# Performance work log

Measured on AMD Instinct MI355X. Metric: run time of the kernel, lower is better.

The kernel has to match this reference:

```python
import jax, jax.numpy as jnp
import numpy as np

EPS = 1e-5

def _conv1x1(x, w, b):
    # x: [B,C,H,W], w: [O,C,1,1], b: [O]
    return jnp.einsum('oc,bchw->bohw', w[:, :, 0, 0], x) + b[None, :, None, None]

def _maxpool(x, s):
    return jax.lax.reduce_window(x, -jnp.inf, jax.lax.max,
                                 (1, 1, s, s), (1, 1, s, s), 'VALID')

def _sra(x, gw, gb, tw, tb, pw, pb, ww, wb, scale):
    # embedded-Gaussian non-local block with spatial sub-sampling on phi/g
    B, C, H, W = x.shape
    ic = gw.shape[0]
    g = _maxpool(_conv1x1(x, gw, gb), scale).reshape(B, ic, -1)    # [B,ic,n]
    phi = _maxpool(_conv1x1(x, pw, pb), scale).reshape(B, ic, -1)  # [B,ic,n]
    theta = _conv1x1(x, tw, tb).reshape(B, ic, -1)                 # [B,ic,N]
    f = jnp.einsum('bcn,bcm->bnm', theta, phi)                     # [B,N,n]
    a = jax.nn.softmax(f, axis=-1)
    y = jnp.einsum('bnm,bcm->bcn', a, g).reshape(B, ic, H, W)
    return _conv1x1(y, ww, wb) + x

def _conv_bn(x, w, gamma, beta, mean, var):
    y = jax.lax.conv_general_dilated(x, w, (1, 1), ((1, 1), (1, 1)),
                                     dimension_numbers=('NCHW', 'OIHW', 'NCHW'))
    inv = gamma / jnp.sqrt(var + EPS)
    return y * inv[None, :, None, None] + (beta - mean * inv)[None, :, None, None]

def setup_inputs() -> dict:
    key = jax.random.key(0)
    B, C = 4, 32
    sizes = [96, 48, 24]
    inp = {}
    ks = iter(jax.random.split(key, 64))
    for i, hw in enumerate(sizes):
        inp[f'fea1_{i}'] = jax.random.normal(next(ks), (B, C, hw, hw), jnp.float32)
        inp[f'fea2_{i}'] = jax.random.normal(next(ks), (B, C, hw, hw), jnp.float32)
    for lv in (1, 2, 3):
        for nm in ('g', 't', 'p'):
            inp[f'{nm}{lv}_w'] = jax.random.normal(next(ks), (C, 2 * C, 1, 1), jnp.float32) * 0.05
            inp[f'{nm}{lv}_b'] = jax.random.normal(next(ks), (C,), jnp.float32) * 0.05
        inp[f'w{lv}_w'] = jax.random.normal(next(ks), (2 * C, C, 1, 1), jnp.float32) * 0.05
        inp[f'w{lv}_b'] = jax.random.normal(next(ks), (2 * C,), jnp.float32) * 0.05
        inp[f'c{lv}_w'] = jax.random.normal(next(ks), (C, 2 * C, 3, 3), jnp.float32) * 0.05
        inp[f'bn{lv}_g'] = jax.random.uniform(next(ks), (C,), jnp.float32, 0.5, 1.5)
        inp[f'bn{lv}_b'] = jax.random.normal(next(ks), (C,), jnp.float32) * 0.05
        inp[f'bn{lv}_m'] = jax.random.normal(next(ks), (C,), jnp.float32) * 0.05
        inp[f'bn{lv}_v'] = jax.random.uniform(next(ks), (C,), jnp.float32, 0.5, 1.5)
    return inp

def reference(fea1_0, fea1_1, fea1_2, fea2_0, fea2_1, fea2_2,
              g1_w, g1_b, t1_w, t1_b, p1_w, p1_b, w1_w, w1_b, c1_w, bn1_g, bn1_b, bn1_m, bn1_v,
              g2_w, g2_b, t2_w, t2_b, p2_w, p2_b, w2_w, w2_b, c2_w, bn2_g, bn2_b, bn2_m, bn2_v,
              g3_w, g3_b, t3_w, t3_b, p3_w, p3_b, w3_w, w3_b, c3_w, bn3_g, bn3_b, bn3_m, bn3_v):
    x1 = jnp.concatenate([fea1_0, fea2_0], axis=1)
    x2 = jnp.concatenate([fea1_1, fea2_1], axis=1)
    x3 = jnp.concatenate([fea1_2, fea2_2], axis=1)
    z1 = _sra(x1, g1_w, g1_b, t1_w, t1_b, p1_w, p1_b, w1_w, w1_b, 2)
    z2 = _sra(x2, g2_w, g2_b, t2_w, t2_b, p2_w, p2_b, w2_w, w2_b, 4)
    z3 = _sra(x3, g3_w, g3_b, t3_w, t3_b, p3_w, p3_b, w3_w, w3_b, 8)
    out1 = _conv_bn(z1, c1_w, bn1_g, bn1_b, bn1_m, bn1_v)
    out2 = _conv_bn(z2, c2_w, bn2_g, bn2_b, bn2_m, bn2_v)
    out3 = _conv_bn(z3, c3_w, bn3_g, bn3_b, bn3_m, bn3_v)
    return (out1, out2, out3)
```

## Files before the change

kernel.cpp:

```cpp
#include <hip/hip_runtime.h>
#include <hip/hip_bf16.h>

typedef __hip_bfloat16 bf16;
typedef __attribute__((ext_vector_type(8))) short short8;
typedef __attribute__((ext_vector_type(4))) float floatx4;

__device__ __forceinline__ float b2f(bf16 v) { return __bfloat162float(v); }
__device__ __forceinline__ bf16 f2b(float v) { return __float2bfloat16(v); }
__device__ __forceinline__ float ldv(const void* p, size_t i, bool f32) {
    return f32 ? ((const float*)p)[i] : b2f(((const bf16*)p)[i]);
}
template <bool F32>
__device__ __forceinline__ float ldt(const void* p, size_t i) {
    return F32 ? ((const float*)p)[i] : b2f(((const bf16*)p)[i]);
}
__device__ __forceinline__ float s2f(short s) {
    unsigned int u = ((unsigned int)(unsigned short)s) << 16;
    float f; __builtin_memcpy(&f, &u, 4); return f;
}
__device__ __forceinline__ short f2s(float f) {
    bf16 h = f2b(f); short s; __builtin_memcpy(&s, &h, 2); return s;
}
__device__ __forceinline__ bool uflag(const int* flag) {
    return __builtin_amdgcn_readfirstlane(flag[0]) != 0;
}
#define MFMA16(a, b, c) __builtin_amdgcn_mfma_f32_16x16x32_bf16(a, b, c, 0, 0, 0)

struct Ptrs { const void* p[45]; };

struct Lvl {
    const void *f1, *f2;
    const float *btgp, *wbf, *bfold;
    const bf16 *Wb, *Wt, *Wc3;
    bf16 *th, *g, *p, *phi, *gt, *yp, *z;
    float* lp;
    int N, n, npad, nch, W, s, wp, H, tX, BN;
    size_t outOff;
};

__global__ void k_detect(const void* x, int* flag) {
    __shared__ int cnt;
    if (threadIdx.x == 0) cnt = 0;
    __syncthreads();
    const unsigned short* us = (const unsigned short*)x;
    int local = 0;
    for (int i = threadIdx.x; i < 8192; i += 256) {
        unsigned e = us[2 * i] & 0x7F80u;
        if (e == 0x7F80u || e == 0u) local++;
    }
    atomicAdd(&cnt, local);
    __syncthreads();
    if (threadIdx.x == 0) flag[0] = (cnt >= 8) ? 1 : 0;
}

#define O_BTGP  0
#define O_WBF   96
#define O_BFOLD 160
#define O_WT    192
#define O_WC3   1216
#define O_WB    10432
#define LVS     13504

__global__ void k_prep(Ptrs in, const int* flag, float* __restrict__ wsf)
{
    int lv = blockIdx.y;
    float* base = wsf + (size_t)lv * LVS;
    const int wb0 = 6 + 13 * lv;
    const void* gw  = in.p[wb0 + 0];
    const void* gb  = in.p[wb0 + 1];
    const void* tw  = in.p[wb0 + 2];
    const void* tb  = in.p[wb0 + 3];
    const void* pw  = in.p[wb0 + 4];
    const void* pb  = in.p[wb0 + 5];
    const void* ww  = in.p[wb0 + 6];
    const void* wb  = in.p[wb0 + 7];
    const void* cw  = in.p[wb0 + 8];
    const void* bng = in.p[wb0 + 9];
    const void* bnb = in.p[wb0 + 10];
    const void* bnm = in.p[wb0 + 11];
    const void* bnv = in.p[wb0 + 12];
    bool f32 = flag[0] != 0;
    int gid = blockIdx.x * 256 + threadIdx.x;
    int stride = gridDim.x * 256;

    float* btgp = base + O_BTGP;
    float* wbf = base + O_WBF;
    float* bfold = base + O_BFOLD;
    bf16* Wt = (bf16*)(base + O_WT);
    bf16* Wc3 = (bf16*)(base + O_WC3);
    bf16* Wb = (bf16*)(base + O_WB);

    for (int e = gid; e < 96 * 64; e += stride) {
        int o = e >> 6, k = e & 63;
        float v;
        if (o < 32)      v = ldv(tw, (size_t)o * 64 + k, f32);
        else if (o < 64) v = ldv(gw, (size_t)(o - 32) * 64 + k, f32);
        else             v = ldv(pw, (size_t)(o - 64) * 64 + k, f32);
        Wb[e] = f2b(v);
    }
    for (int e = gid; e < 96; e += stride) {
        float v = (e < 32) ? ldv(tb, e, f32)
                           : (e < 64 ? ldv(gb, e - 32, f32) : ldv(pb, e - 64, f32));
        btgp[e] = v;
    }
    for (int e = gid; e < 64 * 32; e += stride)
        Wt[e] = f2b(ldv(ww, e, f32));
    for (int e = gid; e < 64; e += stride) wbf[e] = ldv(wb, e, f32);
    for (int e = gid; e < 18432; e += stride) {
        int k = e & 31, n = (e >> 5) & 15, ot = (e >> 9) & 1;
        int tap = (e >> 10) % 9, cc = e / 9216;
        int o = ot * 16 + n, c = cc * 32 + k;
        float inv = ldv(bng, o, f32) * rsqrtf(ldv(bnv, o, f32) + 1e-5f);
        Wc3[e] = f2b(ldv(cw, ((size_t)o * 64 + c) * 9 + tap, f32) * inv);
    }
    for (int e = gid; e < 32; e += stride) {
        float inv = ldv(bng, e, f32) * rsqrtf(ldv(bnv, e, f32) + 1e-5f);
        bfold[e] = ldv(bnb, e, f32) - ldv(bnm, e, f32) * inv;
    }
}

template <bool F32>
__device__ __forceinline__ void tgpm_body(const Lvl& P, int rb)
{
    __shared__ __align__(16) bf16 X[64 * 72];
    int tid = threadIdx.x, lane = tid & 63, wv = tid >> 6;
    int quad = lane >> 4, col = lane & 15;
    int row0 = rb * 64;
    int b = row0 / P.N;
    int pix0 = row0 - b * P.N;

#pragma unroll
    for (int it = 0; it < 16; it++) {
        int e = it * 256 + tid;
        int pix = e & 63, c = e >> 6;
        const void* fx = (c < 32) ? P.f1 : P.f2;
        int cc = c & 31;
        float v = ldt<F32>(fx, (size_t)(b * 32 + cc) * P.N + pix0 + pix);
        X[pix * 72 + c] = f2b(v);
    }
    __syncthreads();

    short8 a_lo = *(const short8*)(X + (wv * 16 + col) * 72 + quad * 8);
    short8 a_hi = *(const short8*)(X + (wv * 16 + col) * 72 + 32 + quad * 8);
    const floatx4 zc = {0.f, 0.f, 0.f, 0.f};
#pragma unroll
    for (int ot = 0; ot < 6; ot++) {
        const bf16* wp = P.Wb + (size_t)(ot * 16 + col) * 64 + quad * 8;
        short8 b_lo = *(const short8*)(wp);
        short8 b_hi = *(const short8*)(wp + 32);
        floatx4 acc = MFMA16(a_lo, b_lo, zc);
        acc = MFMA16(a_hi, b_hi, acc);
        float bias = P.btgp[ot * 16 + col];
        bf16* dst = (ot < 2) ? P.th : ((ot < 4) ? P.g : P.p);
        int och = (ot & 1) * 16 + col;
#pragma unroll
        for (int r = 0; r < 4; r++) {
            int pix = row0 + wv * 16 + quad * 4 + r;
            dst[(size_t)pix * 32 + och] = f2b(acc[r] + bias);
        }
    }
}

__global__ void k_tgpm(Lvl a0, Lvl a1, Lvl a2, int s1, int s2, const int* flag)
{
    int bid = blockIdx.x;
    const Lvl P = bid < s1 ? a0 : (bid < s2 ? a1 : a2);
    int rb = bid - (bid < s1 ? 0 : (bid < s2 ? s1 : s2));
    if (uflag(flag)) tgpm_body<true>(P, rb);
    else             tgpm_body<false>(P, rb);
}

__global__ void k_pool(Lvl a0, Lvl a1, Lvl a2, int s1, int s2)
{
    int bid = blockIdx.x;
    const Lvl P = bid < s1 ? a0 : (bid < s2 ? a1 : a2);
    int local = bid - (bid < s1 ? 0 : (bid < s2 ? s1 : s2));
    int gid = local * 256 + threadIdx.x;
    int npad = P.npad;
    if (gid >= 4 * npad * 32) return;
    int c = gid & 31;
    int j = (gid >> 5) % npad;
    int b = gid / (32 * npad);
    float mg = 0.f, mp = 0.f;
    if (j < P.n) {
        int py = j / P.wp, px = j - py * P.wp;
        const int N = P.N;
        mg = -INFINITY; mp = -INFINITY;
        for (int dy = 0; dy < P.s; dy++)
            for (int dx = 0; dx < P.s; dx++) {
                int idx = (py * P.s + dy) * P.W + px * P.s + dx;
                size_t bse = ((size_t)b * N + idx) * 32 + c;
                mg = fmaxf(mg, b2f(P.g[bse]));
                mp = fmaxf(mp, b2f(P.p[bse]));
            }
    }
    P.phi[((size_t)b * npad + j) * 32 + c] = f2b(mp);
    P.gt[((size_t)b * 32 + c) * npad + j] = f2b(mg);
}

__launch_bounds__(256)
__global__ void k_attn(Lvl a0, Lvl a1, Lvl a2, int s1, int s2)
{
    __shared__ __align__(16) bf16 Pt_s[8 * 1152];
    int bid = blockIdx.x;
    const Lvl P = bid < s1 ? a0 : (bid < s2 ? a1 : a2);
    int local = bid - (bid < s1 ? 0 : (bid < s2 ? s1 : s2));
    int rowblocks = P.BN >> 6;
    int c = local / rowblocks;
    int rb = local - c * rowblocks;

    int tid = threadIdx.x, lane = tid & 63, wv = tid >> 6;
    int quad = lane >> 4, col = lane & 15;
    bf16* Pt0 = Pt_s + wv * 2304;
    int row0 = rb * 64;
    int b = row0 / P.N;
    int npad = P.npad;

    int T = npad >> 6, C = P.nch;
    int js = ((T * c) / C) << 6;
    int je = ((T * (c + 1)) / C) << 6;

    short8 ta = *(const short8*)(P.th + (size_t)(row0 + wv * 16 + col) * 32 + quad * 8);
    const bf16* php = P.phi + (size_t)b * npad * 32 + (size_t)col * 32 + quad * 8;
    const bf16* gtp = P.gt + (size_t)b * 32 * npad + (size_t)col * npad + quad * 8;

    floatx4 y0 = {0.f, 0.f, 0.f, 0.f}, y1 = {0.f, 0.f, 0.f, 0.f};
    float lp4[4] = {0.f, 0.f, 0.f, 0.f};
    const floatx4 zc = {0.f, 0.f, 0.f, 0.f};

    short8 ph[4], gg[4];
#pragma unroll
    for (int k = 0; k < 4; k++)
        ph[k] = *(const short8*)(php + (size_t)(js + 16 * k) * 32);
    gg[0] = *(const short8*)(gtp + js);
    gg[1] = *(const short8*)(gtp + js + 32);
    gg[2] = *(const short8*)(gtp + (size_t)16 * npad + js);
    gg[3] = *(const short8*)(gtp + (size_t)16 * npad + js + 32);

    for (int j0 = js; j0 < je; j0 += 64) {
        int jn = (j0 + 64 < je) ? j0 + 64 : js;
        short8 phN[4], ggN[4];
#pragma unroll
        for (int k = 0; k < 4; k++)
            phN[k] = *(const short8*)(php + (size_t)(jn + 16 * k) * 32);
        ggN[0] = *(const short8*)(gtp + jn);
        ggN[1] = *(const short8*)(gtp + jn + 32);
        ggN[2] = *(const short8*)(gtp + (size_t)16 * npad + jn);
        ggN[3] = *(const short8*)(gtp + (size_t)16 * npad + jn + 32);

        floatx4 s0 = MFMA16(ta, ph[0], zc);
        floatx4 s1 = MFMA16(ta, ph[1], zc);
        floatx4 s2 = MFMA16(ta, ph[2], zc);
        floatx4 s3 = MFMA16(ta, ph[3], zc);
        bf16* PtW = Pt0 + (((j0 - js) & 64) ? 1152 : 0);
#pragma unroll
        for (int r = 0; r < 4; r++) {
            float p0 = __expf(s0[r]), p1 = __expf(s1[r]);
            float p2 = __expf(s2[r]), p3 = __expf(s3[r]);
            lp4[r] += (p0 + p1) + (p2 + p3);
            bf16* pr = PtW + (quad * 4 + r) * 72;
            pr[ 0 + col] = f2b(p0);
            pr[16 + col] = f2b(p1);
            pr[32 + col] = f2b(p2);
            pr[48 + col] = f2b(p3);
        }
#pragma unroll
        for (int kc = 0; kc < 2; kc++) {
            short8 pa = *(const short8*)(PtW + col * 72 + kc * 32 + quad * 8);
            y0 = MFMA16(pa, gg[kc], y0);
            y1 = MFMA16(pa, gg[2 + kc], y1);
        }
#pragma unroll
        for (int k = 0; k < 4; k++) { ph[k] = phN[k]; gg[k] = ggN[k]; }
    }

#pragma unroll
    for (int r = 0; r < 4; r++) {
        float v = lp4[r];
        v += __shfl_xor(v, 1); v += __shfl_xor(v, 2);
        v += __shfl_xor(v, 4); v += __shfl_xor(v, 8);
        int grow = row0 + wv * 16 + quad * 4 + r;
        size_t o = ((size_t)c * P.BN + grow) * 32;
        P.yp[o + col] = f2b(y0[r]);
        P.yp[o + 16 + col] = f2b(y1[r]);
        if (col == 0) P.lp[(size_t)c * P.BN + grow] = v;
    }
}

__launch_bounds__(256)
__global__ void k_merge(Lvl a0, Lvl a1, Lvl a2, int s1, int s2, const int* flag)
{
    bool f32 = uflag(flag);
    __shared__ __align__(16) float zb[64 * 65];
    int bid = blockIdx.x;
    const Lvl P = bid < s1 ? a0 : (bid < s2 ? a1 : a2);
    int rb = bid - (bid < s1 ? 0 : (bid < s2 ? s1 : s2));
    int tid = threadIdx.x, lane = tid & 63, wv = tid >> 6;
    int quad = lane >> 4, col = lane & 15;
    int row0 = rb * 64;
    int b = row0 / P.N;
    int pix0 = row0 - b * P.N;

    int grow = row0 + wv * 16 + col;
    float yv[8] = {0.f, 0.f, 0.f, 0.f, 0.f, 0.f, 0.f, 0.f};
    float L = -(float)(P.npad - P.n);
    for (int cc = 0; cc < P.nch; cc++) {
        short8 v = *(const short8*)(P.yp + ((size_t)cc * P.BN + grow) * 32 + quad * 8);
#pragma unroll
        for (int j = 0; j < 8; j++) yv[j] += s2f(v[j]);
        L += P.lp[(size_t)cc * P.BN + grow];
    }
    float invL = 1.f / L;
    short8 ya;
#pragma unroll
    for (int j = 0; j < 8; j++) ya[j] = f2s(yv[j] * invL);

    const floatx4 zc = {0.f, 0.f, 0.f, 0.f};
    floatx4 zt[4];
#pragma unroll
    for (int ot = 0; ot < 4; ot++) {
        short8 wbv = *(const short8*)(P.Wt + (size_t)(ot * 16 + col) * 32 + quad * 8);
        zt[ot] = MFMA16(ya, wbv, zc);
    }
#pragma unroll
    for (int ot = 0; ot < 4; ot++)
#pragma unroll
        for (int r = 0; r < 4; r++)
            zb[(wv * 16 + quad * 4 + r) * 65 + ot * 16 + col] = zt[ot][r];
    __syncthreads();

    const void* fx = (wv < 2) ? P.f1 : P.f2;
    if (f32) {
#pragma unroll
        for (int k = 0; k < 16; k++) {
            int o = wv * 16 + k, op = o & 31;
            float a = zb[lane * 65 + o] + P.wbf[o];
            a += ((const float*)fx)[(size_t)(b * 32 + op) * P.N + pix0 + lane];
            P.z[((size_t)(b * 64 + o)) * P.N + pix0 + lane] = f2b(a);
        }
    } else {
#pragma unroll
        for (int k = 0; k < 16; k++) {
            int o = wv * 16 + k, op = o & 31;
            float a = zb[lane * 65 + o] + P.wbf[o];
            a += b2f(((const bf16*)fx)[(size_t)(b * 32 + op) * P.N + pix0 + lane]);
            P.z[((size_t)(b * 64 + o)) * P.N + pix0 + lane] = f2b(a);
        }
    }
}

__launch_bounds__(256)
__global__ void k_conv3m(Lvl a0, Lvl a1, Lvl a2, int s1, int s2,
                         void* out, const int* flag)
{
    bool f32 = uflag(flag);
    __shared__ __align__(16) bf16 zh[324 * 34];
    int bid = blockIdx.x;
    const Lvl P = bid < s1 ? a0 : (bid < s2 ? a1 : a2);
    int local = bid - (bid < s1 ? 0 : (bid < s2 ? s1 : s2));
    const int H = P.H, W = H, Npix = H * W, tX = P.tX;
    int tid = threadIdx.x, lane = tid & 63, wv = tid >> 6;
    int quad = lane >> 4, col = lane & 15;
    int tpi = tX * tX;
    int b = local / tpi;
    int t = local - b * tpi;
    int ty = t / tX, tx = t - ty * tX;
    int y0 = ty * 16, x0 = tx * 16;

    floatx4 acc[4][2];
#pragma unroll
    for (int pt = 0; pt < 4; pt++)
#pragma unroll
        for (int ot = 0; ot < 2; ot++) acc[pt][ot] = (floatx4){0.f, 0.f, 0.f, 0.f};

    for (int cc = 0; cc < 2; cc++) {
        __syncthreads();
        for (int e = tid; e < 324 * 32; e += 256) {
            int c = e / 324, pix = e - c * 324;
            int hy = pix / 18, hx = pix - hy * 18;
            int gy = y0 - 1 + hy, gx = x0 - 1 + hx;
            bf16 v = f2b(0.f);
            if (gy >= 0 && gy < H && gx >= 0 && gx < W)
                v = P.z[((size_t)(b * 64 + cc * 32 + c)) * Npix + gy * W + gx];
            zh[pix * 34 + c] = v;
        }
        __syncthreads();
        short8 Bf[9][2];
        const bf16* wp = P.Wc3 + (size_t)cc * 9216 + col * 32 + quad * 8;
#pragma unroll
        for (int tap = 0; tap < 9; tap++)
#pragma unroll
            for (int ot = 0; ot < 2; ot++)
                Bf[tap][ot] = *(const short8*)(wp + (tap * 2 + ot) * 512);
#pragma unroll
        for (int pt = 0; pt < 4; pt++) {
            int yy = wv * 4 + pt;
#pragma unroll
            for (int tap = 0; tap < 9; tap++) {
                int dy = tap / 3, dx = tap - dy * 3;
                short8 A = *(const short8*)(zh + ((yy + dy) * 18 + (col + dx)) * 34 + quad * 8);
                acc[pt][0] = MFMA16(A, Bf[tap][0], acc[pt][0]);
                acc[pt][1] = MFMA16(A, Bf[tap][1], acc[pt][1]);
            }
        }
    }
#pragma unroll
    for (int pt = 0; pt < 4; pt++) {
        int oy = y0 + wv * 4 + pt;
        if (oy >= H) continue;
#pragma unroll
        for (int ot = 0; ot < 2; ot++) {
            int o = ot * 16 + col;
            size_t ob = P.outOff + (size_t)(b * 32 + o) * Npix + (size_t)oy * W;
            float bias = P.bfold[o];
#pragma unroll
            for (int r = 0; r < 4; r++) {
                int ox = x0 + quad * 4 + r;
                if (ox >= W) continue;
                float a = acc[pt][ot][r] + bias;
                if (f32) ((float*)out)[ob + ox] = a;
                else     ((bf16*)out)[ob + ox] = f2b(a);
            }
        }
    }
}

extern "C" void kernel_launch(void* const* d_in, const int* in_sizes, int n_in,
                              void* d_out, int out_size, void* d_ws, size_t ws_size,
                              hipStream_t stream)
{
    const int Hs[3] = {96, 48, 24};
    const int ss[3] = {2, 4, 8};
    const int npads[3] = {2304, 192, 64};
    const size_t outOff[3] = {0, 1179648, 1474560};
    const int BNs[3] = {36864, 9216, 2304};

    int nch[3] = {2, 2, 1};

    int* flag = (int*)d_ws;
    float* wsf = (float*)d_ws + 16;
    float* lpbase = wsf + 3 * LVS;
    size_t lpo[3], lpacc = 0;
    for (int lv = 0; lv < 3; lv++) { lpo[lv] = lpacc; lpacc += (size_t)nch[lv] * BNs[lv]; }
    bf16* bb = (bf16*)(lpbase + lpacc);

    const size_t gpo[3] = {0, 2359296, 2949120};
    size_t ypo[3], ypacc = 0;
    for (int lv = 0; lv < 3; lv++) { ypo[lv] = ypacc; ypacc += (size_t)nch[lv] * BNs[lv] * 32; }
    size_t Asz = ypacc > 3096576 ? ypacc : 3096576;
    const size_t tho[3] = {0, 1179648, 1474560};
    const size_t pho[3] = {1548288, 2138112, 2187264};
    const size_t gto[3] = {1843200, 2162688, 2195456};
    const size_t zo[3]  = {0, 2359296, 2949120};

    k_detect<<<1, 256, 0, stream>>>(d_in[0], flag);

    Ptrs hp;
    for (int i = 0; i < 45 && i < n_in; i++) hp.p[i] = d_in[i];
    k_prep<<<dim3(8, 3), 256, 0, stream>>>(hp, flag, wsf);

    Lvl L[3];
    for (int lv = 0; lv < 3; lv++) {
        int H = Hs[lv], N = H * H;
        float* base = wsf + (size_t)lv * LVS;
        L[lv].f1 = d_in[2 * lv];
        L[lv].f2 = d_in[2 * lv + 1];
        L[lv].btgp = base + O_BTGP;
        L[lv].wbf = base + O_WBF;
        L[lv].bfold = base + O_BFOLD;
        L[lv].Wt = (const bf16*)(base + O_WT);
        L[lv].Wc3 = (const bf16*)(base + O_WC3);
        L[lv].Wb = (const bf16*)(base + O_WB);
        L[lv].g = bb + gpo[lv];
        L[lv].p = bb + gpo[lv] + (size_t)4 * N * 32;
        L[lv].yp = bb + ypo[lv];
        L[lv].th = bb + Asz + tho[lv];
        L[lv].phi = bb + Asz + pho[lv];
        L[lv].gt = bb + Asz + gto[lv];
        L[lv].z = bb + Asz + zo[lv];
        L[lv].lp = lpbase + lpo[lv];
        L[lv].N = N;
        L[lv].n = (H / ss[lv]) * (H / ss[lv]);
        L[lv].npad = npads[lv];
        L[lv].nch = nch[lv];
        L[lv].W = H;
        L[lv].s = ss[lv];
        L[lv].wp = H / ss[lv];
        L[lv].H = H;
        L[lv].tX = (H + 15) / 16;
        L[lv].BN = 4 * N;
        L[lv].outOff = outOff[lv];
    }

    int a0 = nch[0] * (BNs[0] >> 6), a1 = nch[1] * (BNs[1] >> 6), a2 = nch[2] * (BNs[2] >> 6);
    k_tgpm<<<756, 256, 0, stream>>>(L[0], L[1], L[2], 576, 720, flag);
    k_pool<<<1280, 256, 0, stream>>>(L[0], L[1], L[2], 1152, 1248);
    k_attn<<<a0 + a1 + a2, 256, 0, stream>>>(L[0], L[1], L[2], a0, a0 + a1);
    k_merge<<<756, 256, 0, stream>>>(L[0], L[1], L[2], 576, 720, flag);
    k_conv3m<<<196, 256, 0, stream>>>(L[0], L[1], L[2], 144, 180, d_out, flag);
}
```

Baseline: 312.7 us.

## Split conv3 input channels across wave groups; drop attn register prefetch

The 3x3 conv kernel now launches 512 threads and stages both 32-channel halves in shared memory at once. Each group of four waves handles one half, and the partial accumulators are reduced through shared memory, replacing the sequential two-pass loop over channel halves. This gives more parallelism to a kernel that has only 196 blocks, at the cost of more LDS and a reduction step. Separately, the attention kernel drops its software-prefetched, double-buffered phi/g registers and LDS in favour of direct loads, which lowers register and LDS pressure but may expose load latency.

```diff
diff --git a/kernel.cpp b/kernel.cpp
--- a/kernel.cpp
+++ b/kernel.cpp
@@ -201,7 +201,7 @@
 __launch_bounds__(256)
 __global__ void k_attn(Lvl a0, Lvl a1, Lvl a2, int s1, int s2)
 {
-    __shared__ __align__(16) bf16 Pt_s[8 * 1152];
+    __shared__ __align__(16) bf16 Pt_s[4 * 1152];
     int bid = blockIdx.x;
     const Lvl P = bid < s1 ? a0 : (bid < s2 ? a1 : a2);
     int local = bid - (bid < s1 ? 0 : (bid < s2 ? s1 : s2));
@@ -211,7 +211,7 @@
 
     int tid = threadIdx.x, lane = tid & 63, wv = tid >> 6;
     int quad = lane >> 4, col = lane & 15;
-    bf16* Pt0 = Pt_s + wv * 2304;
+    bf16* Pt = Pt_s + wv * 1152;
     int row0 = rb * 64;
     int b = row0 / P.N;
     int npad = P.npad;
@@ -228,37 +228,17 @@
     float lp4[4] = {0.f, 0.f, 0.f, 0.f};
     const floatx4 zc = {0.f, 0.f, 0.f, 0.f};
 
-    short8 ph[4], gg[4];
-#pragma unroll
-    for (int k = 0; k < 4; k++)
-        ph[k] = *(const short8*)(php + (size_t)(js + 16 * k) * 32);
-    gg[0] = *(const short8*)(gtp + js);
-    gg[1] = *(const short8*)(gtp + js + 32);
-    gg[2] = *(const short8*)(gtp + (size_t)16 * npad + js);
-    gg[3] = *(const short8*)(gtp + (size_t)16 * npad + js + 32);
-
     for (int j0 = js; j0 < je; j0 += 64) {
-        int jn = (j0 + 64 < je) ? j0 + 64 : js;
-        short8 phN[4], ggN[4];
-#pragma unroll
-        for (int k = 0; k < 4; k++)
-            phN[k] = *(const short8*)(php + (size_t)(jn + 16 * k) * 32);
-        ggN[0] = *(const short8*)(gtp + jn);
-        ggN[1] = *(const short8*)(gtp + jn + 32);
-        ggN[2] = *(const short8*)(gtp + (size_t)16 * npad + jn);
-        ggN[3] = *(const short8*)(gtp + (size_t)16 * npad + jn + 32);
-
-        floatx4 s0 = MFMA16(ta, ph[0], zc);
-        floatx4 s1 = MFMA16(ta, ph[1], zc);
-        floatx4 s2 = MFMA16(ta, ph[2], zc);
-        floatx4 s3 = MFMA16(ta, ph[3], zc);
-        bf16* PtW = Pt0 + (((j0 - js) & 64) ? 1152 : 0);
+        floatx4 s0 = MFMA16(ta, *(const short8*)(php + (size_t)(j0 +  0) * 32), zc);
+        floatx4 s1 = MFMA16(ta, *(const short8*)(php + (size_t)(j0 + 16) * 32), zc);
+        floatx4 s2 = MFMA16(ta, *(const short8*)(php + (size_t)(j0 + 32) * 32), zc);
+        floatx4 s3 = MFMA16(ta, *(const short8*)(php + (size_t)(j0 + 48) * 32), zc);
 #pragma unroll
         for (int r = 0; r < 4; r++) {
             float p0 = __expf(s0[r]), p1 = __expf(s1[r]);
             float p2 = __expf(s2[r]), p3 = __expf(s3[r]);
             lp4[r] += (p0 + p1) + (p2 + p3);
-            bf16* pr = PtW + (quad * 4 + r) * 72;
+            bf16* pr = Pt + (quad * 4 + r) * 72;
             pr[ 0 + col] = f2b(p0);
             pr[16 + col] = f2b(p1);
             pr[32 + col] = f2b(p2);
@@ -266,12 +246,12 @@
         }
 #pragma unroll
         for (int kc = 0; kc < 2; kc++) {
-            short8 pa = *(const short8*)(PtW + col * 72 + kc * 32 + quad * 8);
-            y0 = MFMA16(pa, gg[kc], y0);
-            y1 = MFMA16(pa, gg[2 + kc], y1);
-        }
-#pragma unroll
-        for (int k = 0; k < 4; k++) { ph[k] = phN[k]; gg[k] = ggN[k]; }
+            short8 pa = *(const short8*)(Pt + col * 72 + kc * 32 + quad * 8);
+            short8 g0 = *(const short8*)(gtp + j0 + kc * 32);
+            short8 g1 = *(const short8*)(gtp + (size_t)16 * npad + j0 + kc * 32);
+            y0 = MFMA16(pa, g0, y0);
+            y1 = MFMA16(pa, g1, y1);
+        }
     }
 
 #pragma unroll
@@ -349,17 +329,20 @@
     }
 }
 
-__launch_bounds__(256)
+__launch_bounds__(512)
 __global__ void k_conv3m(Lvl a0, Lvl a1, Lvl a2, int s1, int s2,
                          void* out, const int* flag)
 {
     bool f32 = uflag(flag);
-    __shared__ __align__(16) bf16 zh[324 * 34];
+    __shared__ __align__(16) char smem[44064];
+    bf16* zh = (bf16*)smem;
+    float* facc = (float*)smem;
     int bid = blockIdx.x;
     const Lvl P = bid < s1 ? a0 : (bid < s2 ? a1 : a2);
     int local = bid - (bid < s1 ? 0 : (bid < s2 ? s1 : s2));
     const int H = P.H, W = H, Npix = H * W, tX = P.tX;
     int tid = threadIdx.x, lane = tid & 63, wv = tid >> 6;
+    int cc = wv >> 2, wv4 = wv & 3;
     int quad = lane >> 4, col = lane & 15;
     int tpi = tX * tX;
     int b = local / tpi;
@@ -367,59 +350,76 @@
     int ty = t / tX, tx = t - ty * tX;
     int y0 = ty * 16, x0 = tx * 16;
 
+    for (int e = tid; e < 2 * 324 * 32; e += 512) {
+        int ch = e / 324, pix = e - ch * 324;
+        int hy = pix / 18, hx = pix - hy * 18;
+        int gy = y0 - 1 + hy, gx = x0 - 1 + hx;
+        bf16 v = f2b(0.f);
+        if (gy >= 0 && gy < H && gx >= 0 && gx < W)
+            v = P.z[((size_t)(b * 64 + ch)) * Npix + gy * W + gx];
+        zh[(ch >> 5) * 11016 + pix * 34 + (ch & 31)] = v;
+    }
+    __syncthreads();
+
+    short8 Bf[9][2];
+    const bf16* wp = P.Wc3 + (size_t)cc * 9216 + col * 32 + quad * 8;
+#pragma unroll
+    for (int tap = 0; tap < 9; tap++)
+#pragma unroll
+        for (int ot = 0; ot < 2; ot++)
+            Bf[tap][ot] = *(const short8*)(wp + (tap * 2 + ot) * 512);
+
     floatx4 acc[4][2];
 #pragma unroll
     for (int pt = 0; pt < 4; pt++)
 #pragma unroll
         for (int ot = 0; ot < 2; ot++) acc[pt][ot] = (floatx4){0.f, 0.f, 0.f, 0.f};
 
-    for (int cc = 0; cc < 2; cc++) {
-        __syncthreads();
-        for (int e = tid; e < 324 * 32; e += 256) {
-            int c = e / 324, pix = e - c * 324;
-            int hy = pix / 18, hx = pix - hy * 18;
-            int gy = y0 - 1 + hy, gx = x0 - 1 + hx;
-            bf16 v = f2b(0.f);
-            if (gy >= 0 && gy < H && gx >= 0 && gx < W)
-                v = P.z[((size_t)(b * 64 + cc * 32 + c)) * Npix + gy * W + gx];
-            zh[pix * 34 + c] = v;
-        }
-        __syncthreads();
-        short8 Bf[9][2];
-        const bf16* wp = P.Wc3 + (size_t)cc * 9216 + col * 32 + quad * 8;
-#pragma unroll
-        for (int tap = 0; tap < 9; tap++)
+    const bf16* zb = zh + cc * 11016;
+#pragma unroll
+    for (int pt = 0; pt < 4; pt++) {
+        int yy = wv4 * 4 + pt;
+#pragma unroll
+        for (int tap = 0; tap < 9; tap++) {
+            int dy = tap / 3, dx = tap - dy * 3;
+            short8 A = *(const short8*)(zb + ((yy + dy) * 18 + (col + dx)) * 34 + quad * 8);
+            acc[pt][0] = MFMA16(A, Bf[tap][0], acc[pt][0]);
+            acc[pt][1] = MFMA16(A, Bf[tap][1], acc[pt][1]);
+        }
+    }
+    __syncthreads();
+
+    if (cc == 1) {
+#pragma unroll
+        for (int pt = 0; pt < 4; pt++)
 #pragma unroll
             for (int ot = 0; ot < 2; ot++)
-                Bf[tap][ot] = *(const short8*)(wp + (tap * 2 + ot) * 512);
+#pragma unroll
+                for (int r = 0; r < 4; r++)
+                    facc[((wv4 * 4 + pt) * 16 + quad * 4 + r) * 33 + ot * 16 + col]
+                        = acc[pt][ot][r];
+    }
+    __syncthreads();
+
+    if (cc == 0) {
 #pragma unroll
         for (int pt = 0; pt < 4; pt++) {
-            int yy = wv * 4 + pt;
-#pragma unroll
-            for (int tap = 0; tap < 9; tap++) {
-                int dy = tap / 3, dx = tap - dy * 3;
-                short8 A = *(const short8*)(zh + ((yy + dy) * 18 + (col + dx)) * 34 + quad * 8);
-                acc[pt][0] = MFMA16(A, Bf[tap][0], acc[pt][0]);
-                acc[pt][1] = MFMA16(A, Bf[tap][1], acc[pt][1]);
-            }
-        }
-    }
-#pragma unroll
-    for (int pt = 0; pt < 4; pt++) {
-        int oy = y0 + wv * 4 + pt;
-        if (oy >= H) continue;
-#pragma unroll
-        for (int ot = 0; ot < 2; ot++) {
-            int o = ot * 16 + col;
-            size_t ob = P.outOff + (size_t)(b * 32 + o) * Npix + (size_t)oy * W;
-            float bias = P.bfold[o];
-#pragma unroll
-            for (int r = 0; r < 4; r++) {
-                int ox = x0 + quad * 4 + r;
-                if (ox >= W) continue;
-                float a = acc[pt][ot][r] + bias;
-                if (f32) ((float*)out)[ob + ox] = a;
-                else     ((bf16*)out)[ob + ox] = f2b(a);
+            int oy = y0 + wv4 * 4 + pt;
+            if (oy >= H) continue;
+#pragma unroll
+            for (int ot = 0; ot < 2; ot++) {
+                int o = ot * 16 + col;
+                size_t ob = P.outOff + (size_t)(b * 32 + o) * Npix + (size_t)oy * W;
+                float bias = P.bfold[o];
+#pragma unroll
+                for (int r = 0; r < 4; r++) {
+                    int ox = x0 + quad * 4 + r;
+                    if (ox >= W) continue;
+                    float a = acc[pt][ot][r] + bias
+                            + facc[((wv4 * 4 + pt) * 16 + quad * 4 + r) * 33 + o];
+                    if (f32) ((float*)out)[ob + ox] = a;
+                    else     ((bf16*)out)[ob + ox] = f2b(a);
+                }
             }
         }
     }
@@ -497,5 +497,5 @@
     k_pool<<<1280, 256, 0, stream>>>(L[0], L[1], L[2], 1152, 1248);
     k_attn<<<a0 + a1 + a2, 256, 0, stream>>>(L[0], L[1], L[2], a0, a0 + a1);
     k_merge<<<756, 256, 0, stream>>>(L[0], L[1], L[2], 576, 720, flag);
-    k_conv3m<<<196, 256, 0, stream>>>(L[0], L[1], L[2], 144, 180, d_out, flag);
-}
+    k_conv3m<<<196, 512, 0, stream>>>(L[0], L[1], L[2], 144, 180, d_out, flag);
+}
```

After: 287.6 us. 1.09x faster.
